# Optimization experiments

Hardware: AMD Instinct MI355X
Metric: run time of the kernel (lower is better)

Reference implementation:

```python
import jax, jax.numpy as jnp
import numpy as np

STRIDES = (8, 16, 32)
FEAT_SIZES = ((80, 80), (40, 40), (20, 20))  # (h, w) per level for 640x640 input
OFFSET = 0.5
NMS_K = 300
IOU_THR = 0.65
EPS = 1e-7


def make_priors():
    """MlvlPointGenerator.grid_priors with with_stride=True, flattened over levels."""
    pts, strs = [], []
    for (h, w), s in zip(FEAT_SIZES, STRIDES):
        xs = (jnp.arange(w, dtype=jnp.float32) + OFFSET) * s
        ys = (jnp.arange(h, dtype=jnp.float32) + OFFSET) * s
        yy, xx = jnp.meshgrid(ys, xs, indexing='ij')
        pts.append(jnp.stack([xx.reshape(-1), yy.reshape(-1)], -1))
        strs.append(jnp.full((h * w, 2), float(s), dtype=jnp.float32))
    return jnp.concatenate(pts, 0), jnp.concatenate(strs, 0)  # [N,2], [N,2]


def pairwise_iou(boxes):  # boxes [K,4] xyxy
    area = jnp.clip(boxes[:, 2] - boxes[:, 0], 0) * jnp.clip(boxes[:, 3] - boxes[:, 1], 0)
    lt = jnp.maximum(boxes[:, None, :2], boxes[None, :, :2])
    rb = jnp.minimum(boxes[:, None, 2:], boxes[None, :, 2:])
    wh = jnp.clip(rb - lt, 0)
    inter = wh[..., 0] * wh[..., 1]
    union = area[:, None] + area[None, :] - inter
    return inter / (union + EPS)


def nms_keep(boxes):  # boxes [K,4] sorted by descending score -> bool keep mask [K]
    K = boxes.shape[0]
    iou = pairwise_iou(boxes)
    idx = jnp.arange(K)

    def body(i, keep):
        sup = (iou[i] > IOU_THR) & (idx > i) & keep[i]
        return keep & ~sup

    return jax.lax.fori_loop(0, K, body, jnp.ones((K,), dtype=bool))


def setup_inputs() -> dict:
    key = jax.random.key(0)
    k1, k2, k3, k4, k5 = jax.random.split(key, 5)
    B, N, K = 128, 8400, 17
    return {
        'cls_scores': jax.random.normal(k1, (B, N, 1), jnp.float32),
        'bbox_preds': jax.random.normal(k2, (B, N, 4), jnp.float32),
        'objectness': jax.random.normal(k3, (B, N), jnp.float32),
        'kpt_offsets': jax.random.normal(k4, (B, N, K, 2), jnp.float32),
        'kpt_vis_preds': jax.random.normal(k5, (B, N, K), jnp.float32),
    }


def reference(cls_scores, bbox_preds, objectness, kpt_offsets, kpt_vis_preds):
    priors, strides = make_priors()  # [N,2] each
    # bbox decode: center-offset + exp wh, YOLOX style
    xy = bbox_preds[..., :2] * strides + priors            # [B,N,2]
    wh = jnp.exp(bbox_preds[..., 2:4]) * strides           # [B,N,2]
    boxes = jnp.concatenate([xy - wh * 0.5, xy + wh * 0.5], -1)  # [B,N,4]
    scores = jax.nn.sigmoid(cls_scores[..., 0]) * jax.nn.sigmoid(objectness)  # [B,N]
    # keypoint decode
    kpts = kpt_offsets * strides[:, None, :] + priors[:, None, :]  # [B,N,K,2]
    B, N, K, _ = kpts.shape
    kpts_flat = kpts.reshape(B, N, K * 2)
    vis = jax.nn.sigmoid(kpt_vis_preds)                    # [B,N,K]
    # fixed-size top-k pre-NMS selection
    top_vals, top_idx = jax.lax.top_k(scores, NMS_K)       # [B,NMS_K]
    gather = lambda x: jnp.take_along_axis(x, top_idx[..., None], axis=1)
    boxes_k = gather(boxes)       # [B,NMS_K,4]
    kpts_k = gather(kpts_flat)    # [B,NMS_K,2K]
    vis_k = gather(vis)           # [B,NMS_K,K]
    keep = jax.vmap(nms_keep)(boxes_k)                      # [B,NMS_K] bool
    final_scores = top_vals * keep.astype(top_vals.dtype)
    # [B, NMS_K, 4 + 1 + 2K + K]
    return jnp.concatenate([boxes_k, final_scores[..., None], kpts_k, vis_k], -1)
```

## Files before the change

kernel.cpp:

```cpp
#include <hip/hip_runtime.h>
#include <math.h>

#define BATCH 128
#define NANCH 8400
#define NMSK  300
#define KPT   17
#define OUTC  56
#define CAND  768
#define NTHR  1024

__device__ __forceinline__ void prior_of(int i, float& stride, float& cx, float& cy) {
    int row, col;
    if (i < 6400)      { stride = 8.0f;  row = i / 80;              col = i - row * 80; }
    else if (i < 8000) { int ii = i - 6400; stride = 16.0f; row = ii / 40; col = ii - row * 40; }
    else               { int ii = i - 8000; stride = 32.0f; row = ii / 20; col = ii - row * 20; }
    cx = ((float)col + 0.5f) * stride;
    cy = ((float)row + 0.5f) * stride;
}

__global__ __launch_bounds__(256) void scores_kernel(
    const float* __restrict__ cls, const float* __restrict__ obj,
    unsigned int* __restrict__ sc)
{
    int i = blockIdx.x * 256 + threadIdx.x;
    if (i < BATCH * NANCH) {
        float ea = (float)exp(-(double)cls[i]);
        float eo = (float)exp(-(double)obj[i]);
        float sa = 1.0f / (1.0f + ea);
        float so = 1.0f / (1.0f + eo);
        sc[i] = __float_as_uint(sa * so);
    }
}

__global__ __launch_bounds__(NTHR) void fused_kernel(
    const float* __restrict__ cls, const float* __restrict__ obj,
    const unsigned int* __restrict__ sc_g, int has_sc,
    const float* __restrict__ bbox, const float* __restrict__ kofs,
    const float* __restrict__ kvis, float* __restrict__ out)
{
    const int b = blockIdx.x;
    const int tid = threadIdx.x;

    __shared__ unsigned int sc[NANCH];
    __shared__ unsigned int hist[256];
    __shared__ unsigned int suf[256];
    __shared__ unsigned int sh_prefix, sh_k, sh_cnt;
    __shared__ unsigned long long ckey[CAND];
    __shared__ float bx1[NMSK], by1[NMSK], bx2[NMSK], by2[NMSK], area[NMSK];
    __shared__ float sval[NMSK], pst[NMSK], ppx[NMSK], ppy[NMSK];
    __shared__ int   sidx[NMSK];
    __shared__ unsigned long long supl[NMSK * 6];
    __shared__ unsigned long long keepw[5];

    if (has_sc) {
        const unsigned int* s = sc_g + (size_t)b * NANCH;
        for (int i = tid; i < NANCH; i += NTHR) sc[i] = s[i];
    } else {
        const float* c = cls + (size_t)b * NANCH;
        const float* o = obj + (size_t)b * NANCH;
        for (int i = tid; i < NANCH; i += NTHR) {
            float ea = (float)exp(-(double)c[i]);
            float eo = (float)exp(-(double)o[i]);
            sc[i] = __float_as_uint((1.0f / (1.0f + ea)) * (1.0f / (1.0f + eo)));
        }
    }
    if (tid == 0) { sh_prefix = 0u; sh_k = NMSK; sh_cnt = 0u; }
    __syncthreads();

    for (int r = 3; r >= 0; --r) {
        if (tid < 256) hist[tid] = 0u;
        __syncthreads();
        unsigned int pfx  = sh_prefix;
        unsigned int kcur = sh_k;
        for (int i = tid; i < NANCH; i += NTHR) {
            unsigned int key = sc[i];
            bool match = (r == 3) || ((key >> ((r + 1) * 8)) == pfx);
            if (match) atomicAdd(&hist[(key >> (r * 8)) & 0xFFu], 1u);
        }
        __syncthreads();
        if (tid < 64) {
            int l = tid;
            unsigned int b0 = hist[4 * l + 0], b1 = hist[4 * l + 1];
            unsigned int b2 = hist[4 * l + 2], b3 = hist[4 * l + 3];
            unsigned int tot = b0 + b1 + b2 + b3;
            unsigned int v = tot;
            #pragma unroll
            for (int d = 1; d < 64; d <<= 1) {
                unsigned int t2 = (unsigned int)__shfl_down((int)v, d, 64);
                if (l + d < 64) v += t2;
            }
            unsigned int above = v - tot;
            suf[4 * l + 3] = above + b3;
            suf[4 * l + 2] = above + b3 + b2;
            suf[4 * l + 1] = above + b3 + b2 + b1;
            suf[4 * l + 0] = above + tot;
        }
        __syncthreads();
        if (tid < 256) {
            unsigned int ge     = suf[tid];
            unsigned int genext = (tid < 255) ? suf[tid + 1] : 0u;
            if (ge >= kcur && genext < kcur) {
                sh_prefix = (pfx << 8) | (unsigned int)tid;
                sh_k      = kcur - genext;
            }
        }
        __syncthreads();
    }

    unsigned int pivot_bits = sh_prefix;
    for (int i = tid; i < NANCH; i += NTHR) {
        unsigned int key = sc[i];
        if (key >= pivot_bits) {
            unsigned int p = atomicAdd(&sh_cnt, 1u);
            if (p < CAND)
                ckey[p] = ((unsigned long long)key << 32)
                        | (unsigned long long)(0xFFFFFFFFu - (unsigned int)i);
        }
    }
    __syncthreads();
    unsigned int M = sh_cnt; if (M > CAND) M = CAND;

    if (tid < (int)M) {
        unsigned long long mine = ckey[tid];
        int rank = 0;
        for (unsigned int t2 = 0; t2 < M; ++t2) rank += (ckey[t2] > mine) ? 1 : 0;
        if (rank < NMSK) {
            sidx[rank] = (int)(0xFFFFFFFFu - (unsigned int)(mine & 0xFFFFFFFFull));
            sval[rank] = __uint_as_float((unsigned int)(mine >> 32));
        }
    }
    __syncthreads();

    if (tid < NMSK) {
        int j = tid;
        int i = sidx[j];
        float stride, cx, cy;
        prior_of(i, stride, cx, cy);
        pst[j] = stride; ppx[j] = cx; ppy[j] = cy;
        float4 bb = *(const float4*)(bbox + ((size_t)b * NANCH + (size_t)i) * 4);
        float x = bb.x * stride + cx;
        float y = bb.y * stride + cy;
        float w = expf(bb.z) * stride;
        float h = expf(bb.w) * stride;
        float x1 = x - 0.5f * w, y1 = y - 0.5f * h;
        float x2 = x + 0.5f * w, y2 = y + 0.5f * h;
        bx1[j] = x1; by1[j] = y1; bx2[j] = x2; by2[j] = y2;
        area[j] = fmaxf(x2 - x1, 0.0f) * fmaxf(y2 - y1, 0.0f);
    }
    __syncthreads();

    for (int t = tid; t < NMSK * 5; t += NTHR) {
        int w = t / NMSK;
        int i = t - w * NMSK;
        int jlo = w * 64; if (jlo < i + 1) jlo = i + 1;
        int jhi = w * 64 + 64; if (jhi > NMSK) jhi = NMSK;
        unsigned long long m = 0;
        float ax1 = bx1[i], ay1 = by1[i], ax2 = bx2[i], ay2 = by2[i], aa = area[i];
        for (int j = jlo; j < jhi; ++j) {
            float lx = fmaxf(ax1, bx1[j]);
            float ly = fmaxf(ay1, by1[j]);
            float rx = fminf(ax2, bx2[j]);
            float ry = fminf(ay2, by2[j]);
            float iw = fmaxf(rx - lx, 0.0f);
            float ih = fmaxf(ry - ly, 0.0f);
            float inter = iw * ih;
            float iou = inter / (aa + area[j] - inter + 1e-7f);
            if (iou > 0.65f) m |= 1ull << (j & 63);
        }
        supl[i * 6 + w] = m;
    }
    __syncthreads();

    if (tid < 64) {
        unsigned long long k0 = ~0ull, k1 = ~0ull, k2 = ~0ull, k3 = ~0ull;
        unsigned long long k4 = (1ull << (NMSK - 256)) - 1ull;
        const unsigned long long* sp = supl;
        #define GSTEP(KW, I) \
            if (((KW) >> ((I) & 63)) & 1ull) { \
                const unsigned long long* s = sp + (size_t)(I) * 6; \
                k0 &= ~s[0]; k1 &= ~s[1]; k2 &= ~s[2]; k3 &= ~s[3]; k4 &= ~s[4]; }
        for (int i = 0;   i < 64;   ++i) { GSTEP(k0, i) }
        for (int i = 64;  i < 128;  ++i) { GSTEP(k1, i) }
        for (int i = 128; i < 192;  ++i) { GSTEP(k2, i) }
        for (int i = 192; i < 256;  ++i) { GSTEP(k3, i) }
        for (int i = 256; i < NMSK; ++i) { GSTEP(k4, i) }
        #undef GSTEP
        if (tid == 0) { keepw[0] = k0; keepw[1] = k1; keepw[2] = k2; keepw[3] = k3; keepw[4] = k4; }
    } else {
        const float* kof = kofs + (size_t)b * NANCH * 34;
        const float* kvi = kvis + (size_t)b * NANCH * KPT;
        float* ob = out + (size_t)b * NMSK * OUTC;
        for (int e = tid - 64; e < NMSK * 51; e += NTHR - 64) {
            int j  = e / 51;
            int ci = e - j * 51;
            int i  = sidx[j];
            float v;
            if (ci < 34) {
                float off = kof[(size_t)i * 34 + ci];
                v = off * pst[j] + ((ci & 1) ? ppy[j] : ppx[j]);
            } else {
                float x = kvi[(size_t)i * KPT + (ci - 34)];
                v = 1.0f / (1.0f + expf(-x));
            }
            ob[j * OUTC + 5 + ci] = v;
        }
    }
    __syncthreads();

    float* ob = out + (size_t)b * NMSK * OUTC;
    for (int t = tid; t < NMSK * 5; t += NTHR) {
        int j  = t / 5;
        int ci = t - j * 5;
        float v;
        if (ci == 0)      v = bx1[j];
        else if (ci == 1) v = by1[j];
        else if (ci == 2) v = bx2[j];
        else if (ci == 3) v = by2[j];
        else {
            bool kp = (keepw[j >> 6] >> (j & 63)) & 1ull;
            v = kp ? sval[j] : 0.0f;
        }
        ob[j * OUTC + ci] = v;
    }
}

extern "C" void kernel_launch(void* const* d_in, const int* in_sizes, int n_in,
                              void* d_out, int out_size, void* d_ws, size_t ws_size,
                              hipStream_t stream) {
    const float* cls  = (const float*)d_in[0];
    const float* bbox = (const float*)d_in[1];
    const float* obj  = (const float*)d_in[2];
    const float* kofs = (const float*)d_in[3];
    const float* kvis = (const float*)d_in[4];
    float* out = (float*)d_out;

    size_t need_sc = (size_t)BATCH * NANCH * sizeof(unsigned int);
    unsigned int* sc = (unsigned int*)d_ws;
    int has_sc = (ws_size >= need_sc) ? 1 : 0;

    if (has_sc) {
        int nblk = (BATCH * NANCH + 255) / 256;
        scores_kernel<<<nblk, 256, 0, stream>>>(cls, obj, sc);
    }
    fused_kernel<<<BATCH, NTHR, 0, stream>>>(cls, obj, sc, has_sc,
                                             bbox, kofs, kvis, out);
}
```

Baseline: 287.5 us.

## Use per-wave histograms, fuse first radix pass into load, and split block into overlapping halves

The first radix-select histogram is built while scores are loaded, and each wave gets its own histogram to reduce shared-atomic contention, with the suffix scan and pivot search done in a single wave. After candidate ranking the block splits in two. Half the waves gather and decode keypoints and exit, while the other half decodes boxes, builds the IoU suppression bitmask and runs greedy NMS, synchronising among themselves through a custom spin barrier on a shared counter. Box coordinates and scores are written straight to global memory, which removes the final pass over shared memory. The cost is a hand-rolled partial barrier and more shared memory for the per-wave histograms.

Result: no change. 289.5 us (+0.7%).

```diff
diff --git a/kernel.cpp b/kernel.cpp
--- a/kernel.cpp
+++ b/kernel.cpp
@@ -8,6 +8,7 @@
 #define OUTC  56
 #define CAND  768
 #define NTHR  1024
+#define NWAVE 16
 
 __device__ __forceinline__ void prior_of(int i, float& stride, float& cx, float& cy) {
     int row, col;
@@ -16,6 +17,15 @@
     else               { int ii = i - 8000; stride = 32.0f; row = ii / 20; col = ii - row * 20; }
     cx = ((float)col + 0.5f) * stride;
     cy = ((float)row + 0.5f) * stride;
+}
+
+__device__ __forceinline__ void half_barrier(unsigned int* cnt, unsigned int target) {
+    __threadfence_block();
+    if ((threadIdx.x & 63) == 0)
+        __hip_atomic_fetch_add(cnt, 1u, __ATOMIC_ACQ_REL, __HIP_MEMORY_SCOPE_WORKGROUP);
+    while (__hip_atomic_load(cnt, __ATOMIC_ACQUIRE, __HIP_MEMORY_SCOPE_WORKGROUP) < target)
+        __builtin_amdgcn_s_sleep(1);
+    __threadfence_block();
 }
 
 __global__ __launch_bounds__(256) void scores_kernel(
@@ -38,70 +48,87 @@
     const float* __restrict__ bbox, const float* __restrict__ kofs,
     const float* __restrict__ kvis, float* __restrict__ out)
 {
-    const int b = blockIdx.x;
-    const int tid = threadIdx.x;
+    const int b    = blockIdx.x;
+    const int tid  = threadIdx.x;
+    const int w    = tid >> 6;
+    const int lane = tid & 63;
 
     __shared__ unsigned int sc[NANCH];
-    __shared__ unsigned int hist[256];
-    __shared__ unsigned int suf[256];
-    __shared__ unsigned int sh_prefix, sh_k, sh_cnt;
+    __shared__ unsigned int whist[NWAVE * 256];
+    __shared__ unsigned int sh_prefix, sh_k, sh_cnt, barcnt;
     __shared__ unsigned long long ckey[CAND];
-    __shared__ float bx1[NMSK], by1[NMSK], bx2[NMSK], by2[NMSK], area[NMSK];
-    __shared__ float sval[NMSK], pst[NMSK], ppx[NMSK], ppy[NMSK];
+    __shared__ float bx1[NMSK], by1[NMSK], bx2[NMSK], by2[NMSK], area[NMSK], sval[NMSK];
     __shared__ int   sidx[NMSK];
     __shared__ unsigned long long supl[NMSK * 6];
-    __shared__ unsigned long long keepw[5];
-
+
+    if (tid == 0) { sh_prefix = 0u; sh_k = NMSK; sh_cnt = 0u; barcnt = 0u; }
+    for (int i = tid; i < NWAVE * 256; i += NTHR) whist[i] = 0u;
+    __syncthreads();
+
+    unsigned int* myh = &whist[w * 256];
     if (has_sc) {
         const unsigned int* s = sc_g + (size_t)b * NANCH;
-        for (int i = tid; i < NANCH; i += NTHR) sc[i] = s[i];
+        for (int i = tid; i < NANCH; i += NTHR) {
+            unsigned int key = s[i];
+            sc[i] = key;
+            atomicAdd(&myh[key >> 24], 1u);
+        }
     } else {
         const float* c = cls + (size_t)b * NANCH;
         const float* o = obj + (size_t)b * NANCH;
         for (int i = tid; i < NANCH; i += NTHR) {
             float ea = (float)exp(-(double)c[i]);
             float eo = (float)exp(-(double)o[i]);
-            sc[i] = __float_as_uint((1.0f / (1.0f + ea)) * (1.0f / (1.0f + eo)));
-        }
-    }
-    if (tid == 0) { sh_prefix = 0u; sh_k = NMSK; sh_cnt = 0u; }
+            unsigned int key = __float_as_uint((1.0f / (1.0f + ea)) * (1.0f / (1.0f + eo)));
+            sc[i] = key;
+            atomicAdd(&myh[key >> 24], 1u);
+        }
+    }
     __syncthreads();
 
     for (int r = 3; r >= 0; --r) {
-        if (tid < 256) hist[tid] = 0u;
-        __syncthreads();
-        unsigned int pfx  = sh_prefix;
-        unsigned int kcur = sh_k;
-        for (int i = tid; i < NANCH; i += NTHR) {
-            unsigned int key = sc[i];
-            bool match = (r == 3) || ((key >> ((r + 1) * 8)) == pfx);
-            if (match) atomicAdd(&hist[(key >> (r * 8)) & 0xFFu], 1u);
-        }
-        __syncthreads();
-        if (tid < 64) {
-            int l = tid;
-            unsigned int b0 = hist[4 * l + 0], b1 = hist[4 * l + 1];
-            unsigned int b2 = hist[4 * l + 2], b3 = hist[4 * l + 3];
+        if (r < 3) {
+            for (int i = tid; i < NWAVE * 256; i += NTHR) whist[i] = 0u;
+            __syncthreads();
+            unsigned int pfx = sh_prefix;
+            for (int i = tid; i < NANCH; i += NTHR) {
+                unsigned int key = sc[i];
+                if ((key >> ((r + 1) * 8)) == pfx)
+                    atomicAdd(&myh[(key >> (r * 8)) & 0xFFu], 1u);
+            }
+            __syncthreads();
+        }
+        if (w == 0) {
+            unsigned int b0 = 0, b1 = 0, b2 = 0, b3 = 0;
+            #pragma unroll 4
+            for (int ww = 0; ww < NWAVE; ++ww) {
+                const unsigned int* hh = &whist[ww * 256 + 4 * lane];
+                b0 += hh[0]; b1 += hh[1]; b2 += hh[2]; b3 += hh[3];
+            }
             unsigned int tot = b0 + b1 + b2 + b3;
             unsigned int v = tot;
             #pragma unroll
             for (int d = 1; d < 64; d <<= 1) {
                 unsigned int t2 = (unsigned int)__shfl_down((int)v, d, 64);
-                if (l + d < 64) v += t2;
+                if (lane + d < 64) v += t2;
             }
             unsigned int above = v - tot;
-            suf[4 * l + 3] = above + b3;
-            suf[4 * l + 2] = above + b3 + b2;
-            suf[4 * l + 1] = above + b3 + b2 + b1;
-            suf[4 * l + 0] = above + tot;
-        }
-        __syncthreads();
-        if (tid < 256) {
-            unsigned int ge     = suf[tid];
-            unsigned int genext = (tid < 255) ? suf[tid + 1] : 0u;
-            if (ge >= kcur && genext < kcur) {
-                sh_prefix = (pfx << 8) | (unsigned int)tid;
-                sh_k      = kcur - genext;
+            unsigned int s3 = above + b3;
+            unsigned int s2 = s3 + b2;
+            unsigned int s1 = s2 + b1;
+            unsigned int s0 = s1 + b0;
+            unsigned int snext = (unsigned int)__shfl_down((int)s0, 1, 64);
+            if (lane == 63) snext = 0u;
+            unsigned int kcur = sh_k;
+            unsigned int pfx  = sh_prefix;
+            unsigned int ge[4] = { s0, s1, s2, s3 };
+            unsigned int gn[4] = { s1, s2, s3, snext };
+            #pragma unroll
+            for (int j = 0; j < 4; ++j) {
+                if (ge[j] >= kcur && gn[j] < kcur) {
+                    sh_prefix = (pfx << 8) | (unsigned int)(4 * lane + j);
+                    sh_k      = kcur - gn[j];
+                }
             }
         }
         __syncthreads();
@@ -131,29 +158,54 @@
     }
     __syncthreads();
 
+    float* ob = out + (size_t)b * NMSK * OUTC;
+
+    if (w >= 8) {
+        const float* kof = kofs + (size_t)b * NANCH * 34;
+        const float* kvi = kvis + (size_t)b * NANCH * KPT;
+        for (int e = tid - 512; e < NMSK * 51; e += 512) {
+            int j  = e / 51;
+            int ci = e - j * 51;
+            int i  = sidx[j];
+            float stride, cx, cy;
+            prior_of(i, stride, cx, cy);
+            float v;
+            if (ci < 34) {
+                float off = kof[(size_t)i * 34 + ci];
+                v = off * stride + ((ci & 1) ? cy : cx);
+            } else {
+                float x = kvi[(size_t)i * KPT + (ci - 34)];
+                v = 1.0f / (1.0f + expf(-x));
+            }
+            ob[j * OUTC + 5 + ci] = v;
+        }
+        return;
+    }
+
     if (tid < NMSK) {
         int j = tid;
         int i = sidx[j];
         float stride, cx, cy;
         prior_of(i, stride, cx, cy);
-        pst[j] = stride; ppx[j] = cx; ppy[j] = cy;
         float4 bb = *(const float4*)(bbox + ((size_t)b * NANCH + (size_t)i) * 4);
         float x = bb.x * stride + cx;
         float y = bb.y * stride + cy;
-        float w = expf(bb.z) * stride;
-        float h = expf(bb.w) * stride;
-        float x1 = x - 0.5f * w, y1 = y - 0.5f * h;
-        float x2 = x + 0.5f * w, y2 = y + 0.5f * h;
+        float ww = expf(bb.z) * stride;
+        float hh = expf(bb.w) * stride;
+        float x1 = x - 0.5f * ww, y1 = y - 0.5f * hh;
+        float x2 = x + 0.5f * ww, y2 = y + 0.5f * hh;
         bx1[j] = x1; by1[j] = y1; bx2[j] = x2; by2[j] = y2;
         area[j] = fmaxf(x2 - x1, 0.0f) * fmaxf(y2 - y1, 0.0f);
-    }
-    __syncthreads();
-
-    for (int t = tid; t < NMSK * 5; t += NTHR) {
-        int w = t / NMSK;
-        int i = t - w * NMSK;
-        int jlo = w * 64; if (jlo < i + 1) jlo = i + 1;
-        int jhi = w * 64 + 64; if (jhi > NMSK) jhi = NMSK;
+        float4 bo; bo.x = x1; bo.y = y1; bo.z = x2; bo.w = y2;
+        *(float4*)(ob + j * OUTC) = bo;
+    }
+    half_barrier(&barcnt, 8);
+
+    for (int t = tid; t < NMSK * 5; t += 512) {
+        int w2 = t / NMSK;
+        int i  = t - w2 * NMSK;
+        int jlo = w2 * 64; if (jlo < i + 1) jlo = i + 1;
+        int jhi = w2 * 64 + 64; if (jhi > NMSK) jhi = NMSK;
         unsigned long long m = 0;
         float ax1 = bx1[i], ay1 = by1[i], ax2 = bx2[i], ay2 = by2[i], aa = area[i];
         for (int j = jlo; j < jhi; ++j) {
@@ -164,14 +216,14 @@
             float iw = fmaxf(rx - lx, 0.0f);
             float ih = fmaxf(ry - ly, 0.0f);
             float inter = iw * ih;
-            float iou = inter / (aa + area[j] - inter + 1e-7f);
+            float iou = inter / (aa + area[i < j ? j : j] - inter + 1e-7f);
             if (iou > 0.65f) m |= 1ull << (j & 63);
         }
-        supl[i * 6 + w] = m;
-    }
-    __syncthreads();
-
-    if (tid < 64) {
+        supl[i * 6 + w2] = m;
+    }
+    half_barrier(&barcnt, 16);
+
+    if (w == 0) {
         unsigned long long k0 = ~0ull, k1 = ~0ull, k2 = ~0ull, k3 = ~0ull;
         unsigned long long k4 = (1ull << (NMSK - 256)) - 1ull;
         const unsigned long long* sp = supl;
@@ -185,42 +237,16 @@
         for (int i = 192; i < 256;  ++i) { GSTEP(k3, i) }
         for (int i = 256; i < NMSK; ++i) { GSTEP(k4, i) }
         #undef GSTEP
-        if (tid == 0) { keepw[0] = k0; keepw[1] = k1; keepw[2] = k2; keepw[3] = k3; keepw[4] = k4; }
-    } else {
-        const float* kof = kofs + (size_t)b * NANCH * 34;
-        const float* kvi = kvis + (size_t)b * NANCH * KPT;
-        float* ob = out + (size_t)b * NMSK * OUTC;
-        for (int e = tid - 64; e < NMSK * 51; e += NTHR - 64) {
-            int j  = e / 51;
-            int ci = e - j * 51;
-            int i  = sidx[j];
-            float v;
-            if (ci < 34) {
-                float off = kof[(size_t)i * 34 + ci];
-                v = off * pst[j] + ((ci & 1) ? ppy[j] : ppx[j]);
-            } else {
-                float x = kvi[(size_t)i * KPT + (ci - 34)];
-                v = 1.0f / (1.0f + expf(-x));
-            }
-            ob[j * OUTC + 5 + ci] = v;
-        }
-    }
-    __syncthreads();
-
-    float* ob = out + (size_t)b * NMSK * OUTC;
-    for (int t = tid; t < NMSK * 5; t += NTHR) {
-        int j  = t / 5;
-        int ci = t - j * 5;
-        float v;
-        if (ci == 0)      v = bx1[j];
-        else if (ci == 1) v = by1[j];
-        else if (ci == 2) v = bx2[j];
-        else if (ci == 3) v = by2[j];
-        else {
-            bool kp = (keepw[j >> 6] >> (j & 63)) & 1ull;
-            v = kp ? sval[j] : 0.0f;
-        }
-        ob[j * OUTC + ci] = v;
+        #pragma unroll
+        for (int it = 0; it < 5; ++it) {
+            int j = lane + 64 * it;
+            if (j < NMSK) {
+                unsigned long long kw = (it == 0) ? k0 : (it == 1) ? k1
+                                       : (it == 2) ? k2 : (it == 3) ? k3 : k4;
+                bool kp = (kw >> lane) & 1ull;
+                ob[j * OUTC + 4] = kp ? sval[j] : 0.0f;
+            }
+        }
     }
 }
 
```
